# Kernel optimization log

Measured on AMD Instinct MI355X. Metric: run time of the kernel, lower is better.

## Reference

```python
import jax, jax.numpy as jnp
import numpy as np

EPS = 1e-5

def _pw1d(W, b, x):  # W (O,C), x (B,C,N) -> (B,O,N); 1x1 Conv1d
    return jnp.einsum('oc,bcn->bon', W, x) + b[None, :, None]

def _pw2d(W, b, x):  # W (O,C), x (B,C,N,K) -> (B,O,N,K); 1x1 Conv2d
    return jnp.einsum('oc,bcnk->bonk', W, x) + b[None, :, None, None]

def _bn(x, g, b, m, v):  # BatchNorm2d, eval mode, over channel axis 1
    scale = g / jnp.sqrt(v + EPS)
    return (x - m[None, :, None, None]) * scale[None, :, None, None] + b[None, :, None, None]

def _knn(pos, k):  # pos (B,3,N) -> idx (B,N,K) of nearest neighbors (incl. self)
    p = jnp.transpose(pos, (0, 2, 1))             # (B,N,3)
    sq = jnp.sum(p * p, axis=-1)                  # (B,N)
    d = sq[:, :, None] - 2.0 * jnp.einsum('bid,bjd->bij', p, p) + sq[:, None, :]
    _, idx = jax.lax.top_k(-d, k)
    return idx

def _gather(feat, idx):  # feat (B,C,N), idx (B,N,K) -> (B,C,N,K)
    return jax.vmap(lambda f, i: f[:, i])(feat, idx)


def setup_inputs() -> dict:
    key = jax.random.key(0)
    B, C, N, H, AH, K = 4, 64, 4096, 64, 256, 16
    ks = jax.random.split(key, 32)
    s = lambda i, shp, sc=0.05: jax.random.normal(ks[i], shp, dtype=jnp.float32) * sc
    u = lambda i, shp: jax.random.uniform(ks[i], shp, dtype=jnp.float32, minval=0.5, maxval=1.5)
    return {
        'x': jax.random.normal(ks[0], (B, 3, N), dtype=jnp.float32),
        'y': jax.random.normal(ks[1], (B, C, N), dtype=jnp.float32),
        'W_start': s(2, (C, C)), 'b_start': s(3, (C,)),
        'W_key': s(4, (C, C)), 'b_key': s(5, (C,)),
        'W_query': s(6, (C, 3)), 'b_query': s(7, (C,)),
        'P1': s(8, (H, 3)), 'pb1': s(9, (H,)),
        'bn1_g': u(10, (H,)), 'bn1_b': s(11, (H,)), 'bn1_m': s(12, (H,)), 'bn1_v': u(13, (H,)),
        'P2': s(14, (C, H)), 'pb2': s(15, (C,)),
        'A1': s(16, (AH, C)), 'ab1': s(17, (AH,)),
        'bn2_g': u(18, (AH,)), 'bn2_b': s(19, (AH,)), 'bn2_m': s(20, (AH,)), 'bn2_v': u(21, (AH,)),
        'A2': s(22, (C, AH)), 'ab2': s(23, (C,)),
        'W_end': s(24, (C, C)), 'b_end': s(25, (C,)),
        'n_knn': 16,
    }


def reference(x, y, W_start, b_start, W_key, b_key, W_query, b_query,
              P1, pb1, bn1_g, bn1_b, bn1_m, bn1_v, P2, pb2,
              A1, ab1, bn2_g, bn2_b, bn2_m, bn2_v, A2, ab2,
              W_end, b_end, n_knn):
    identity = y
    y1 = _pw1d(W_start, b_start, y)                 # linear_start, (B,C,N)
    idx = _knn(x, n_knn)                            # (B,N,K)
    key = _pw1d(W_key, b_key, y1)
    value = y1
    query = _pw1d(W_query, b_query, x)              # 3 -> C pointwise
    key_g = _gather(key, idx)                       # (B,C,N,K)
    qk_rel = query[..., None] - key_g
    pos_rel = x[..., None] - _gather(x, idx)        # (B,3,N,K)
    pe = _pw2d(P2, pb2, jax.nn.relu(_bn(_pw2d(P1, pb1, pos_rel), bn1_g, bn1_b, bn1_m, bn1_v)))
    attn = _pw2d(A2, ab2, jax.nn.relu(_bn(_pw2d(A1, ab1, qk_rel + pe), bn2_g, bn2_b, bn2_m, bn2_v)))
    attn = jax.nn.softmax(attn, axis=-1)            # softmax over neighbor axis
    val = value[..., None] + pe                     # (B,C,N,K)
    agg = jnp.sum(attn * val, axis=-1)              # einsum 'bcij,bcij->bci'
    out = _pw1d(W_end, b_end, agg) + identity
    return out
```

## Files before the change

### kernel.cpp

```cpp
#include <hip/hip_runtime.h>
#include <hip/hip_bf16.h>

#define BB 4
#define CC 64
#define NN 4096
#define HH 64
#define AH 256
#define KNN 16
#define EPSV 1e-5f

#define KNN_BLKS 2048
#define PF_BLKS 256
#define PP_BLKS 32

typedef __attribute__((ext_vector_type(8))) short short8;
typedef __attribute__((ext_vector_type(4))) short short4v;
typedef __attribute__((ext_vector_type(4))) unsigned short ushort4v;
typedef __attribute__((ext_vector_type(4))) float floatx4;

__device__ __forceinline__ unsigned short f2bf(float f) {
    unsigned u = __float_as_uint(f);
    u += 0x7FFFu + ((u >> 16) & 1u);
    return (unsigned short)(u >> 16);
}
__device__ __forceinline__ float bf2f(unsigned short u) {
    return __uint_as_float(((unsigned)u) << 16);
}
__device__ __forceinline__ unsigned pkbf(float a, float b) {
    __hip_bfloat162 h = __float22bfloat162_rn(make_float2(a, b));
    return *(reinterpret_cast<unsigned*>(&h));
}
__device__ __forceinline__ unsigned long long umin64(unsigned long long a, unsigned long long b) {
    return a < b ? a : b;
}
__device__ __forceinline__ unsigned long long umax64(unsigned long long a, unsigned long long b) {
    return a > b ? a : b;
}
__device__ __forceinline__ unsigned long long shfl_xor_u64(unsigned long long v, int m) {
    int lo = __shfl_xor((int)(unsigned)(v & 0xFFFFFFFFull), m);
    int hi = __shfl_xor((int)(unsigned)(v >> 32), m);
    return ((unsigned long long)(unsigned)hi << 32) | (unsigned)lo;
}
__device__ __forceinline__ unsigned fmono(float d) {
    unsigned u = __float_as_uint(d);
    return ((int)u < 0) ? ~u : (u | 0x80000000u);
}

#define UPITCH 68
#define HPITCH 68

__device__ __forceinline__ short8 lds_frag(const unsigned short* p) {
    short4v lo = *(const short4v*)p;
    short4v hi = *(const short4v*)(p + 4);
    short8 v;
    v[0] = lo[0]; v[1] = lo[1]; v[2] = lo[2]; v[3] = lo[3];
    v[4] = hi[0]; v[5] = hi[1]; v[6] = hi[2]; v[7] = hi[3];
    return v;
}

__global__ __launch_bounds__(256, 3) void fused_prep_knn(
    const float* __restrict__ x, const float* __restrict__ y,
    const float* __restrict__ Ws, const float* __restrict__ bs,
    const float* __restrict__ Wk, const float* __restrict__ bk,
    const float* __restrict__ Wq, const float* __restrict__ bq,
    const float* __restrict__ P1, const float* __restrict__ pb1,
    const float* __restrict__ P2, const float* __restrict__ A1,
    const float* __restrict__ ab1, const float* __restrict__ A2,
    const float* __restrict__ g1, const float* __restrict__ b1v,
    const float* __restrict__ m1, const float* __restrict__ v1,
    const float* __restrict__ g2, const float* __restrict__ b2v,
    const float* __restrict__ m2, const float* __restrict__ v2,
    const float* __restrict__ Wend,
    int* __restrict__ idx_out,
    unsigned short* __restrict__ y1bf, unsigned short* __restrict__ keybf,
    unsigned short* __restrict__ qrybf,
    unsigned short* __restrict__ A1L, unsigned short* __restrict__ A2L,
    unsigned short* __restrict__ P2L, unsigned short* __restrict__ WendL,
    float* __restrict__ P1p, float* __restrict__ ab1f, float* __restrict__ bn2s_c) {
    __shared__ __align__(16) char smem[49152];
    int blk = blockIdx.x;
    int lane = threadIdx.x & 63;
    int w = threadIdx.x >> 6;

    if (blk < KNN_BLKS) {
        float* px = (float*)smem;
        float* py = px + NN;
        float* pz = py + NN;
        unsigned long long* surv = (unsigned long long*)smem;

        int b = blk >> 9;
        int grp = blk & 511;
        const float* xb = x + (size_t)b * 3 * NN;
        for (int i = threadIdx.x; i < NN; i += 256) {
            px[i] = xb[i];
            py[i] = xb[NN + i];
            pz[i] = xb[2 * NN + i];
        }
        __syncthreads();

        int n0 = (grp << 3) + (w << 1);
        float q0x = px[n0], q0y = py[n0], q0z = pz[n0];
        float q1x = px[n0 + 1], q1y = py[n0 + 1], q1z = pz[n0 + 1];
        float q0w = q0x * q0x + q0y * q0y + q0z * q0z;
        float q1w = q1x * q1x + q1y * q1y + q1z * q1z;
        q0x *= -2.f; q0y *= -2.f; q0z *= -2.f;
        q1x *= -2.f; q1y *= -2.f; q1z *= -2.f;

        float d0reg[64], d1reg[64];
        float vmin0 = 3.4e38f, vmin1 = 3.4e38f;
#pragma unroll
        for (int r = 0; r < 16; ++r) {
            int c = r * 64 + lane;
            float4 cx = ((const float4*)px)[c];
            float4 cy = ((const float4*)py)[c];
            float4 cz = ((const float4*)pz)[c];
            float exv[4] = {cx.x, cx.y, cx.z, cx.w};
            float eyv[4] = {cy.x, cy.y, cy.z, cy.w};
            float ezv[4] = {cz.x, cz.y, cz.z, cz.w};
#pragma unroll
            for (int e = 0; e < 4; ++e) {
                float nx = exv[e], ny = eyv[e], nz = ezv[e];
                float nc = nx * nx + ny * ny + nz * nz;
                float d0 = fmaf(q0x, nx, fmaf(q0y, ny, fmaf(q0z, nz, nc + q0w)));
                float d1 = fmaf(q1x, nx, fmaf(q1y, ny, fmaf(q1z, nz, nc + q1w)));
                d0reg[r * 4 + e] = d0;
                d1reg[r * 4 + e] = d1;
                vmin0 = fminf(vmin0, d0);
                vmin1 = fminf(vmin1, d1);
            }
        }

        float T[2];
#pragma unroll
        for (int t = 0; t < 2; ++t) {
            float v = t ? vmin1 : vmin0;
#pragma unroll
            for (int k = 2; k <= 64; k <<= 1) {
#pragma unroll
                for (int j = k >> 1; j > 0; j >>= 1) {
                    float o = __shfl_xor(v, j);
                    bool lower = (lane & j) == 0;
                    bool up = (lane & k) == 0;
                    float mn = fminf(v, o), mx = fmaxf(v, o);
                    v = (lower == up) ? mn : mx;
                }
            }
            T[t] = __shfl(v, 15);
        }
        __syncthreads();

#pragma unroll
        for (int t = 0; t < 2; ++t) {
            float Tt = T[t];
            unsigned long long* buf = surv + (((w << 1) + t) << 7);
            unsigned cnt = 0;
#pragma unroll
            for (int s = 0; s < 64; ++s) {
                float d = t ? d1reg[s] : d0reg[s];
                bool hit = d <= Tt;
                unsigned long long mask = __ballot(hit);
                if (hit) {
                    unsigned off = cnt + (unsigned)__popcll(mask & ((1ull << lane) - 1ull));
                    if (off < 128) {
                        int j = ((s >> 2) * 64 + lane) * 4 + (s & 3);
                        buf[off] = ((unsigned long long)fmono(d) << 32) | (unsigned)j;
                    }
                }
                cnt += (unsigned)__popcll(mask);
            }
            if (cnt > 128) cnt = 128;

            unsigned long long v0 = (lane < (int)cnt) ? buf[lane] : 0xFFFFFFFFFFFFFFFFull;
            if (cnt <= 64) {
#pragma unroll
                for (int k = 2; k <= 64; k <<= 1) {
#pragma unroll
                    for (int j = k >> 1; j > 0; j >>= 1) {
                        bool lower = (lane & j) == 0;
                        bool up = (lane & k) == 0;
                        unsigned long long o0 = shfl_xor_u64(v0, j);
                        v0 = (lower == up) ? umin64(v0, o0) : umax64(v0, o0);
                    }
                }
            } else {
                unsigned long long v1 = (lane + 64 < (int)cnt) ? buf[lane + 64]
                                                               : 0xFFFFFFFFFFFFFFFFull;
#pragma unroll
                for (int k = 2; k <= 128; k <<= 1) {
#pragma unroll
                    for (int j = k >> 1; j > 0; j >>= 1) {
                        if (j >= 64) {
                            unsigned long long lo = umin64(v0, v1), hi = umax64(v0, v1);
                            v0 = lo; v1 = hi;
                        } else {
                            bool lower = (lane & j) == 0;
                            unsigned long long o0 = shfl_xor_u64(v0, j);
                            bool up0 = ((lane & k) == 0);
                            v0 = (lower == up0) ? umin64(v0, o0) : umax64(v0, o0);
                            unsigned long long o1 = shfl_xor_u64(v1, j);
                            bool up1 = (((64 + lane) & k) == 0);
                            v1 = (lower == up1) ? umin64(v1, o1) : umax64(v1, o1);
                        }
                    }
                }
            }
            if (lane < KNN)
                idx_out[((size_t)b * NN + n0 + t) * KNN + lane] =
                    (int)(unsigned)(v0 & 0xFFFFFFFFull);
        }
    } else if (blk < KNN_BLKS + PF_BLKS) {
        unsigned short* tl = (unsigned short*)smem + w * 16 * UPITCH;
        int g4 = (blk - KNN_BLKS) * 4 + w;
        int b = g4 >> 8;
        int n0 = (g4 & 255) << 4;
        int m = lane & 15, quad = lane >> 4;
        size_t ybase = (size_t)b * CC * NN;

        short8 yA[2];
#pragma unroll
        for (int ks = 0; ks < 2; ++ks)
#pragma unroll
            for (int j = 0; j < 8; j += 2) {
                float a = y[ybase + (size_t)(ks * 32 + quad * 8 + j) * NN + n0 + m];
                float bq2 = y[ybase + (size_t)(ks * 32 + quad * 8 + j + 1) * NN + n0 + m];
                ((unsigned*)&yA[ks])[j >> 1] = pkbf(a, bq2);
            }

#pragma unroll
        for (int ot = 0; ot < 4; ++ot) {
            short8 bb0, bb1;
#pragma unroll
            for (int ks = 0; ks < 2; ++ks) {
                const float* wr = Ws + (ot * 16 + m) * CC + ks * 32 + quad * 8;
                float4 lo = *(const float4*)wr;
                float4 hi = *(const float4*)(wr + 4);
                short8 bb;
                ((unsigned*)&bb)[0] = pkbf(lo.x, lo.y);
                ((unsigned*)&bb)[1] = pkbf(lo.z, lo.w);
                ((unsigned*)&bb)[2] = pkbf(hi.x, hi.y);
                ((unsigned*)&bb)[3] = pkbf(hi.z, hi.w);
                if (ks == 0) bb0 = bb; else bb1 = bb;
            }
            floatx4 acc = (floatx4){0.f, 0.f, 0.f, 0.f};
            acc = __builtin_amdgcn_mfma_f32_16x16x32_bf16(yA[0], bb0, acc, 0, 0, 0);
            acc = __builtin_amdgcn_mfma_f32_16x16x32_bf16(yA[1], bb1, acc, 0, 0, 0);
            float bsv = bs[ot * 16 + m];
#pragma unroll
            for (int r = 0; r < 4; r += 2) {
                unsigned p2 = pkbf(acc[r] + bsv, acc[r + 1] + bsv);
                tl[(4 * quad + r) * UPITCH + ot * 16 + m] = (unsigned short)p2;
                tl[(4 * quad + r + 1) * UPITCH + ot * 16 + m] = (unsigned short)(p2 >> 16);
            }
        }
        __syncthreads();

        short8 uA[2];
#pragma unroll
        for (int ks = 0; ks < 2; ++ks)
            uA[ks] = lds_frag(&tl[m * UPITCH + ks * 32 + quad * 8]);

        int p = lane >> 2, ck = lane & 3;
        size_t obase = ((size_t)b * NN + n0 + p) * CC + ck * 16;
#pragma unroll
        for (int s = 0; s < 4; ++s)
            *(ushort4v*)(y1bf + obase + s * 4) =
                *(const ushort4v*)&tl[p * UPITCH + ck * 16 + s * 4];
        __syncthreads();

#pragma unroll
        for (int ot = 0; ot < 4; ++ot) {
            short8 bb0, bb1;
#pragma unroll
            for (int ks = 0; ks < 2; ++ks) {
                const float* wr = Wk + (ot * 16 + m) * CC + ks * 32 + quad * 8;
                float4 lo = *(const float4*)wr;
                float4 hi = *(const float4*)(wr + 4);
                short8 bb;
                ((unsigned*)&bb)[0] = pkbf(lo.x, lo.y);
                ((unsigned*)&bb)[1] = pkbf(lo.z, lo.w);
                ((unsigned*)&bb)[2] = pkbf(hi.x, hi.y);
                ((unsigned*)&bb)[3] = pkbf(hi.z, hi.w);
                if (ks == 0) bb0 = bb; else bb1 = bb;
            }
            floatx4 acc = (floatx4){0.f, 0.f, 0.f, 0.f};
            acc = __builtin_amdgcn_mfma_f32_16x16x32_bf16(uA[0], bb0, acc, 0, 0, 0);
            acc = __builtin_amdgcn_mfma_f32_16x16x32_bf16(uA[1], bb1, acc, 0, 0, 0);
            float bkv = bk[ot * 16 + m];
#pragma unroll
            for (int r = 0; r < 4; r += 2) {
                unsigned p2 = pkbf(acc[r] + bkv, acc[r + 1] + bkv);
                tl[(4 * quad + r) * UPITCH + ot * 16 + m] = (unsigned short)p2;
                tl[(4 * quad + r + 1) * UPITCH + ot * 16 + m] = (unsigned short)(p2 >> 16);
            }
        }
        __syncthreads();
#pragma unroll
        for (int s = 0; s < 4; ++s)
            *(ushort4v*)(keybf + obase + s * 4) =
                *(const ushort4v*)&tl[p * UPITCH + ck * 16 + s * 4];

        float x0 = x[(size_t)(b * 3 + 0) * NN + n0 + p];
        float x1 = x[(size_t)(b * 3 + 1) * NN + n0 + p];
        float x2 = x[(size_t)(b * 3 + 2) * NN + n0 + p];
#pragma unroll
        for (int s = 0; s < 4; ++s) {
            ushort4v pk;
#pragma unroll
            for (int e = 0; e < 4; ++e) {
                int ch = ck * 16 + s * 4 + e;
                pk[e] = f2bf(Wq[3 * ch + 0] * x0 + Wq[3 * ch + 1] * x1 +
                             Wq[3 * ch + 2] * x2 + bq[ch]);
            }
            *(ushort4v*)(qrybf + obase + s * 4) = pk;
        }
    } else {
        int pb = blk - KNN_BLKS - PF_BLKS;
        int t0 = threadIdx.x;
        int t = pb * 256 + t0;
        const int stride = PP_BLKS * 256;
        if (pb == 0) {
            if (t0 < HH) {
                float s = g1[t0] * rsqrtf(v1[t0] + EPSV);
                float c = b1v[t0] - m1[t0] * s;
                P1p[4 * t0 + 0] = P1[3 * t0 + 0] * s;
                P1p[4 * t0 + 1] = P1[3 * t0 + 1] * s;
                P1p[4 * t0 + 2] = P1[3 * t0 + 2] * s;
                P1p[4 * t0 + 3] = pb1[t0] * s + c;
            }
            if (t0 < AH) {
                float s = g2[t0] * rsqrtf(v2[t0] + EPSV);
                bn2s_c[t0] = s;
                ab1f[t0] = ab1[t0] * s + (b2v[t0] - m2[t0] * s);
            }
        }
        for (int i = t; i < 16384; i += stride) {
            int e = i & 7, ln = (i >> 3) & 63, ks = (i >> 9) & 1, ht = i >> 10;
            int m = ln & 15, q = ln >> 4;
            int h = ht * 16 + m;
            float s = g2[h] * rsqrtf(v2[h] + EPSV);
            A1L[i] = f2bf(A1[h * CC + ks * 32 + q * 8 + e] * s);
        }
        for (int i = t; i < 16384; i += stride) {
            int e = i & 7, ln = (i >> 3) & 63, kk = (i >> 9) & 7, nt = i >> 12;
            int m = ln & 15, q = ln >> 4;
            A2L[i] = f2bf(A2[(nt * 16 + m) * AH + kk * 32 + q * 8 + e]);
        }
        for (int i = t; i < 4096; i += stride) {
            int e = i & 7, ln = (i >> 3) & 63, ks = (i >> 9) & 1, nt = i >> 10;
            int m = ln & 15, q = ln >> 4;
            P2L[i] = f2bf(P2[(nt * 16 + m) * HH + ks * 32 + q * 8 + e]);
        }
        for (int i = t; i < 4096; i += stride) {
            int e = i & 7, ln = (i >> 3) & 63, ks = (i >> 9) & 1, wv = i >> 10;
            int m = ln & 15, q = ln >> 4;
            WendL[i] = f2bf(Wend[(wv * 16 + m) * CC + ks * 32 + q * 8 + e]);
        }
    }
}

__global__ __launch_bounds__(256, 3) void attn_mfma(
    const float* __restrict__ x, const float* __restrict__ y,
    const unsigned short* __restrict__ y1bf, const unsigned short* __restrict__ keybf,
    const unsigned short* __restrict__ qrybf, const int* __restrict__ idx,
    const float* __restrict__ P1p, const unsigned short* __restrict__ P2L,
    const float* __restrict__ pb2, const unsigned short* __restrict__ A1L,
    const float* __restrict__ ab1f, const float* __restrict__ bn2s_c,
    const unsigned short* __restrict__ A2L, const unsigned short* __restrict__ WendL,
    const float* __restrict__ bend,
    float* __restrict__ out) {
    __shared__ unsigned short u_lds[128 * UPITCH];
    __shared__ unsigned short hid_lds[128 * HPITCH];
    __shared__ float agg_lds[8 * 68];
    __shared__ float outstage[512];

    int blk = blockIdx.x;
    int b = blk & 3;
    int n0 = (blk >> 2) << 3;
    int w = threadIdx.x >> 6;
    int lane = threadIdx.x & 63;
    int m = lane & 15, quad = lane >> 4;

    int pt[2];
    size_t bpt[2];
#pragma unroll
    for (int t = 0; t < 2; ++t) {
        pt[t] = n0 + 2 * w + t;
        bpt[t] = (size_t)b * NN + pt[t];
    }

    int jm[2], j4[2][4];
    unsigned short qu[2][4], kvu[2][4][4], y1u[2][4];
#pragma unroll
    for (int t = 0; t < 2; ++t) {
        jm[t] = idx[bpt[t] * KNN + m];
#pragma unroll
        for (int r = 0; r < 4; ++r) j4[t][r] = idx[bpt[t] * KNN + 4 * quad + r];
#pragma unroll
        for (int nt = 0; nt < 4; ++nt) {
            qu[t][nt] = qrybf[bpt[t] * CC + nt * 16 + m];
            y1u[t][nt] = y1bf[bpt[t] * CC + nt * 16 + m];
#pragma unroll
            for (int r = 0; r < 4; ++r)
                kvu[t][nt][r] = keybf[((size_t)b * NN + j4[t][r]) * CC + nt * 16 + m];
        }
    }

    short8 h1A[2][2];
#pragma unroll
    for (int t = 0; t < 2; ++t) {
        float dx = x[(size_t)(b * 3 + 0) * NN + pt[t]] - x[(size_t)(b * 3 + 0) * NN + jm[t]];
        float dy = x[(size_t)(b * 3 + 1) * NN + pt[t]] - x[(size_t)(b * 3 + 1) * NN + jm[t]];
        float dz = x[(size_t)(b * 3 + 2) * NN + pt[t]] - x[(size_t)(b * 3 + 2) * NN + jm[t]];
#pragma unroll
        for (int ks = 0; ks < 2; ++ks)
#pragma unroll
            for (int j = 0; j < 8; j += 2) {
                int h1 = ks * 32 + quad * 8 + j;
                const float4 p0 = *(const float4*)(P1p + 4 * h1);
                const float4 p1 = *(const float4*)(P1p + 4 * h1 + 4);
                float a0 = fmaxf(p0.x * dx + p0.y * dy + p0.z * dz + p0.w, 0.f);
                float a1 = fmaxf(p1.x * dx + p1.y * dy + p1.z * dz + p1.w, 0.f);
                ((unsigned*)&h1A[t][ks])[j >> 1] = pkbf(a0, a1);
            }
    }

    floatx4 pacc[2][4];
#pragma unroll
    for (int t = 0; t < 2; ++t)
#pragma unroll
        for (int nt = 0; nt < 4; ++nt) pacc[t][nt] = (floatx4){0.f, 0.f, 0.f, 0.f};
#pragma unroll
    for (int ks = 0; ks < 2; ++ks)
#pragma unroll
        for (int nt = 0; nt < 4; ++nt) {
            short8 bb = *(const short8*)(P2L + ((nt * 2 + ks) * 64 + lane) * 8);
            pacc[0][nt] = __builtin_amdgcn_mfma_f32_16x16x32_bf16(h1A[0][ks], bb, pacc[0][nt], 0, 0, 0);
            pacc[1][nt] = __builtin_amdgcn_mfma_f32_16x16x32_bf16(h1A[1][ks], bb, pacc[1][nt], 0, 0, 0);
        }
#pragma unroll
    for (int nt = 0; nt < 4; ++nt) {
        float pb = pb2[nt * 16 + m];
#pragma unroll
        for (int t = 0; t < 2; ++t)
#pragma unroll
            for (int r = 0; r < 4; ++r) pacc[t][nt][r] += pb;
    }

#pragma unroll
    for (int t = 0; t < 2; ++t)
#pragma unroll
        for (int nt = 0; nt < 4; ++nt) {
            float qv = bf2f(qu[t][nt]);
            float u0 = qv - bf2f(kvu[t][nt][0]) + pacc[t][nt][0];
            float u1 = qv - bf2f(kvu[t][nt][1]) + pacc[t][nt][1];
            float u2 = qv - bf2f(kvu[t][nt][2]) + pacc[t][nt][2];
            float u3 = qv - bf2f(kvu[t][nt][3]) + pacc[t][nt][3];
            unsigned p01 = pkbf(u0, u1), p23 = pkbf(u2, u3);
            int base = (w * 32 + t * 16 + 4 * quad) * UPITCH + nt * 16 + m;
            u_lds[base + 0 * UPITCH] = (unsigned short)p01;
            u_lds[base + 1 * UPITCH] = (unsigned short)(p01 >> 16);
            u_lds[base + 2 * UPITCH] = (unsigned short)p23;
            u_lds[base + 3 * UPITCH] = (unsigned short)(p23 >> 16);
        }

    short8 uA[2][2];
#pragma unroll
    for (int t = 0; t < 2; ++t)
#pragma unroll
        for (int ks = 0; ks < 2; ++ks)
            uA[t][ks] = lds_frag(&u_lds[(w * 32 + t * 16 + m) * UPITCH + ks * 32 + quad * 8]);

    floatx4 acc2[2][4];
#pragma unroll
    for (int t = 0; t < 2; ++t)
#pragma unroll
        for (int nt = 0; nt < 4; ++nt) acc2[t][nt] = (floatx4){0.f, 0.f, 0.f, 0.f};

    for (int qd = 0; qd < 4; ++qd) {
#pragma unroll
        for (int nt4 = 0; nt4 < 4; ++nt4) {
            int ht = qd * 4 + nt4;
            const unsigned short* a1t = A1L + ht * 1024 + lane * 8;
            short8 b0 = *(const short8*)(a1t);
            short8 b1 = *(const short8*)(a1t + 512);
            int h = ht * 16 + m;
            float t0 = ab1f[h];
#pragma unroll
            for (int t = 0; t < 2; ++t) {
                floatx4 acc = (floatx4){0.f, 0.f, 0.f, 0.f};
                acc = __builtin_amdgcn_mfma_f32_16x16x32_bf16(uA[t][0], b0, acc, 0, 0, 0);
                acc = __builtin_amdgcn_mfma_f32_16x16x32_bf16(uA[t][1], b1, acc, 0, 0, 0);
                float h0 = fmaxf(acc[0] + t0, 0.f);
                float h1 = fmaxf(acc[1] + t0, 0.f);
                float h2 = fmaxf(acc[2] + t0, 0.f);
                float h3 = fmaxf(acc[3] + t0, 0.f);
                unsigned p01 = pkbf(h0, h1), p23 = pkbf(h2, h3);
                int base = (w * 32 + t * 16 + 4 * quad) * HPITCH + nt4 * 16 + m;
                hid_lds[base + 0 * HPITCH] = (unsigned short)p01;
                hid_lds[base + 1 * HPITCH] = (unsigned short)(p01 >> 16);
                hid_lds[base + 2 * HPITCH] = (unsigned short)p23;
                hid_lds[base + 3 * HPITCH] = (unsigned short)(p23 >> 16);
            }
        }
        short8 hA[2][2];
#pragma unroll
        for (int t = 0; t < 2; ++t)
#pragma unroll
            for (int ks = 0; ks < 2; ++ks)
                hA[t][ks] = lds_frag(&hid_lds[(w * 32 + t * 16 + m) * HPITCH + ks * 32 + quad * 8]);
#pragma unroll
        for (int ks = 0; ks < 2; ++ks)
#pragma unroll
            for (int nt = 0; nt < 4; ++nt) {
                int kk = qd * 2 + ks;
                short8 bb = *(const short8*)(A2L + ((nt * 8 + kk) * 64 + lane) * 8);
                acc2[0][nt] = __builtin_amdgcn_mfma_f32_16x16x32_bf16(hA[0][ks], bb, acc2[0][nt], 0, 0, 0);
                acc2[1][nt] = __builtin_amdgcn_mfma_f32_16x16x32_bf16(hA[1][ks], bb, acc2[1][nt], 0, 0, 0);
            }
    }

#pragma unroll
    for (int t = 0; t < 2; ++t)
#pragma unroll
        for (int nt = 0; nt < 4; ++nt) {
            float l0 = acc2[t][nt][0], l1 = acc2[t][nt][1];
            float l2 = acc2[t][nt][2], l3 = acc2[t][nt][3];
            float mx = fmaxf(fmaxf(l0, l1), fmaxf(l2, l3));
            mx = fmaxf(mx, __shfl_xor(mx, 16));
            mx = fmaxf(mx, __shfl_xor(mx, 32));
            float e0 = __expf(l0 - mx), e1 = __expf(l1 - mx);
            float e2 = __expf(l2 - mx), e3 = __expf(l3 - mx);
            float sum = (e0 + e1) + (e2 + e3);
            sum += __shfl_xor(sum, 16);
            sum += __shfl_xor(sum, 32);
            float y1v = bf2f(y1u[t][nt]);
            float contrib = e0 * (y1v + pacc[t][nt][0]) + e1 * (y1v + pacc[t][nt][1]) +
                            e2 * (y1v + pacc[t][nt][2]) + e3 * (y1v + pacc[t][nt][3]);
            contrib += __shfl_xor(contrib, 16);
            contrib += __shfl_xor(contrib, 32);
            float agg = contrib / sum;
            if (quad == 0) agg_lds[(2 * w + t) * 68 + nt * 16 + m] = agg;
        }
    __syncthreads();

    short8 aggA[2];
#pragma unroll
    for (int ks = 0; ks < 2; ++ks)
#pragma unroll
        for (int j = 0; j < 8; j += 2) {
            float a0 = agg_lds[(m & 7) * 68 + ks * 32 + quad * 8 + j];
            float a1 = agg_lds[(m & 7) * 68 + ks * 32 + quad * 8 + j + 1];
            ((unsigned*)&aggA[ks])[j >> 1] = pkbf(a0, a1);
        }
    short8 wb0 = *(const short8*)(WendL + ((w * 2 + 0) * 64 + lane) * 8);
    short8 wb1 = *(const short8*)(WendL + ((w * 2 + 1) * 64 + lane) * 8);
    floatx4 facc = (floatx4){0.f, 0.f, 0.f, 0.f};
    facc = __builtin_amdgcn_mfma_f32_16x16x32_bf16(aggA[0], wb0, facc, 0, 0, 0);
    facc = __builtin_amdgcn_mfma_f32_16x16x32_bf16(aggA[1], wb1, facc, 0, 0, 0);
    if (quad < 2) {
        float be = bend[w * 16 + m];
#pragma unroll
        for (int r = 0; r < 4; ++r)
            outstage[(w * 16 + m) * 8 + 4 * quad + r] = facc[r] + be;
    }
    __syncthreads();

    int t2 = threadIdx.x;
    int o = t2 >> 2, pp = (t2 & 3) * 2;
#pragma unroll
    for (int e = 0; e < 2; ++e) {
        size_t oi = ((size_t)(b * CC + o)) * NN + n0 + pp + e;
        out[oi] = outstage[o * 8 + pp + e] + y[oi];
    }
}

extern "C" void kernel_launch(void* const* d_in, const int* in_sizes, int n_in,
                              void* d_out, int out_size, void* d_ws, size_t ws_size,
                              hipStream_t stream) {
    const float* x    = (const float*)d_in[0];
    const float* y    = (const float*)d_in[1];
    const float* Ws   = (const float*)d_in[2];
    const float* bs   = (const float*)d_in[3];
    const float* Wk   = (const float*)d_in[4];
    const float* bk   = (const float*)d_in[5];
    const float* Wq   = (const float*)d_in[6];
    const float* bq   = (const float*)d_in[7];
    const float* P1   = (const float*)d_in[8];
    const float* pb1  = (const float*)d_in[9];
    const float* g1   = (const float*)d_in[10];
    const float* b1   = (const float*)d_in[11];
    const float* m1   = (const float*)d_in[12];
    const float* v1   = (const float*)d_in[13];
    const float* P2   = (const float*)d_in[14];
    const float* pb2  = (const float*)d_in[15];
    const float* A1   = (const float*)d_in[16];
    const float* ab1  = (const float*)d_in[17];
    const float* g2   = (const float*)d_in[18];
    const float* b2   = (const float*)d_in[19];
    const float* m2   = (const float*)d_in[20];
    const float* v2   = (const float*)d_in[21];
    const float* A2   = (const float*)d_in[22];
    const float* ab2  = (const float*)d_in[23];
    const float* Wend = (const float*)d_in[24];
    const float* bend = (const float*)d_in[25];
    (void)ab2;

    unsigned short* usws = (unsigned short*)d_ws;
    unsigned short* y1bf  = usws;
    unsigned short* keybf = usws + 1048576;
    unsigned short* qrybf = usws + 2097152;
    int* idx = (int*)(usws + 3145728);
    unsigned short* A1L = usws + 3670016;
    unsigned short* A2L = A1L + 16384;
    unsigned short* P2L = A2L + 16384;
    unsigned short* WendL = P2L + 4096;
    float* P1p   = (float*)(WendL + 4096);
    float* ab1f  = P1p + 256;
    float* bn2sc = ab1f + 256;
    float* out   = (float*)d_out;

    hipLaunchKernelGGL(fused_prep_knn, dim3(KNN_BLKS + PF_BLKS + PP_BLKS), dim3(256), 0, stream,
                       x, y, Ws, bs, Wk, bk, Wq, bq,
                       P1, pb1, P2, A1, ab1, A2,
                       g1, b1, m1, v1, g2, b2, m2, v2, Wend,
                       idx, y1bf, keybf, qrybf,
                       A1L, A2L, P2L, WendL, P1p, ab1f, bn2sc);
    hipLaunchKernelGGL(attn_mfma, dim3(2048), dim3(256), 0, stream,
                       x, y, y1bf, keybf, qrybf, idx,
                       P1p, P2L, pb2, A1L, ab1f, bn2sc, A2L, WendL,
                       bend, out);
}
```

Before: 195.4 us.

## Interleave channel layout for vectorized neighbor gathers and fold log2e into softmax

Stores y1, key and query in a permuted channel order (g*4+nt holds channel nt*16+g). Each lane's four channels become contiguous, so the attention kernel gathers neighbor keys and loads query and y1 with one 8-byte vector load instead of four scalar 2-byte loads. This targets the cost of the random-access key gather. Separately, it pre-scales A2 by log2(e) so the softmax can use exp2f directly; the per-channel bias cancels over the neighbor axis, so the result is unchanged. The risk is that any unseen consumer of these buffers that assumes the old channel order would now read wrong data.

```diff
diff --git a/kernel.cpp b/kernel.cpp
--- a/kernel.cpp
+++ b/kernel.cpp
@@ -8,6 +8,7 @@
 #define AH 256
 #define KNN 16
 #define EPSV 1e-5f
+#define LOG2E 1.44269504088896f
 
 #define KNN_BLKS 2048
 #define PF_BLKS 256
@@ -57,6 +58,7 @@
     v[4] = hi[0]; v[5] = hi[1]; v[6] = hi[2]; v[7] = hi[3];
     return v;
 }
+
 
 __global__ __launch_bounds__(256, 3) void fused_prep_knn(
     const float* __restrict__ x, const float* __restrict__ y,
@@ -259,12 +261,17 @@
         for (int ks = 0; ks < 2; ++ks)
             uA[ks] = lds_frag(&tl[m * UPITCH + ks * 32 + quad * 8]);
 
-        int p = lane >> 2, ck = lane & 3;
-        size_t obase = ((size_t)b * NN + n0 + p) * CC + ck * 16;
-#pragma unroll
-        for (int s = 0; s < 4; ++s)
-            *(ushort4v*)(y1bf + obase + s * 4) =
-                *(const ushort4v*)&tl[p * UPITCH + ck * 16 + s * 4];
+        int p = lane >> 2, gb = lane & 3;
+        size_t obase = ((size_t)b * NN + n0 + p) * 64;
+#pragma unroll
+        for (int s = 0; s < 4; ++s) {
+            int g = gb * 4 + s;
+            ushort4v pk;
+#pragma unroll
+            for (int nt = 0; nt < 4; ++nt)
+                pk[nt] = tl[p * UPITCH + nt * 16 + g];
+            *(ushort4v*)(y1bf + obase + g * 4) = pk;
+        }
         __syncthreads();
 
 #pragma unroll
@@ -295,23 +302,29 @@
         }
         __syncthreads();
 #pragma unroll
-        for (int s = 0; s < 4; ++s)
-            *(ushort4v*)(keybf + obase + s * 4) =
-                *(const ushort4v*)&tl[p * UPITCH + ck * 16 + s * 4];
+        for (int s = 0; s < 4; ++s) {
+            int g = gb * 4 + s;
+            ushort4v pk;
+#pragma unroll
+            for (int nt = 0; nt < 4; ++nt)
+                pk[nt] = tl[p * UPITCH + nt * 16 + g];
+            *(ushort4v*)(keybf + obase + g * 4) = pk;
+        }
 
         float x0 = x[(size_t)(b * 3 + 0) * NN + n0 + p];
         float x1 = x[(size_t)(b * 3 + 1) * NN + n0 + p];
         float x2 = x[(size_t)(b * 3 + 2) * NN + n0 + p];
 #pragma unroll
         for (int s = 0; s < 4; ++s) {
+            int g = gb * 4 + s;
             ushort4v pk;
 #pragma unroll
-            for (int e = 0; e < 4; ++e) {
-                int ch = ck * 16 + s * 4 + e;
-                pk[e] = f2bf(Wq[3 * ch + 0] * x0 + Wq[3 * ch + 1] * x1 +
-                             Wq[3 * ch + 2] * x2 + bq[ch]);
-            }
-            *(ushort4v*)(qrybf + obase + s * 4) = pk;
+            for (int nt = 0; nt < 4; ++nt) {
+                int ch = nt * 16 + g;
+                pk[nt] = f2bf(Wq[3 * ch + 0] * x0 + Wq[3 * ch + 1] * x1 +
+                              Wq[3 * ch + 2] * x2 + bq[ch]);
+            }
+            *(ushort4v*)(qrybf + obase + g * 4) = pk;
         }
     } else {
         int pb = blk - KNN_BLKS - PF_BLKS;
@@ -343,7 +356,7 @@
         for (int i = t; i < 16384; i += stride) {
             int e = i & 7, ln = (i >> 3) & 63, kk = (i >> 9) & 7, nt = i >> 12;
             int m = ln & 15, q = ln >> 4;
-            A2L[i] = f2bf(A2[(nt * 16 + m) * AH + kk * 32 + q * 8 + e]);
+            A2L[i] = f2bf(A2[(nt * 16 + m) * AH + kk * 32 + q * 8 + e] * LOG2E);
         }
         for (int i = t; i < 4096; i += stride) {
             int e = i & 7, ln = (i >> 3) & 63, ks = (i >> 9) & 1, nt = i >> 10;
@@ -389,20 +402,17 @@
     }
 
     int jm[2], j4[2][4];
-    unsigned short qu[2][4], kvu[2][4][4], y1u[2][4];
+    ushort4v qu4[2], y14[2], kv4[2][4];
 #pragma unroll
     for (int t = 0; t < 2; ++t) {
         jm[t] = idx[bpt[t] * KNN + m];
 #pragma unroll
         for (int r = 0; r < 4; ++r) j4[t][r] = idx[bpt[t] * KNN + 4 * quad + r];
-#pragma unroll
-        for (int nt = 0; nt < 4; ++nt) {
-            qu[t][nt] = qrybf[bpt[t] * CC + nt * 16 + m];
-            y1u[t][nt] = y1bf[bpt[t] * CC + nt * 16 + m];
-#pragma unroll
-            for (int r = 0; r < 4; ++r)
-                kvu[t][nt][r] = keybf[((size_t)b * NN + j4[t][r]) * CC + nt * 16 + m];
-        }
+        qu4[t] = *(const ushort4v*)(qrybf + bpt[t] * 64 + m * 4);
+        y14[t] = *(const ushort4v*)(y1bf + bpt[t] * 64 + m * 4);
+#pragma unroll
+        for (int r = 0; r < 4; ++r)
+            kv4[t][r] = *(const ushort4v*)(keybf + ((size_t)b * NN + j4[t][r]) * 64 + m * 4);
     }
 
     short8 h1A[2][2];
@@ -450,11 +460,11 @@
     for (int t = 0; t < 2; ++t)
 #pragma unroll
         for (int nt = 0; nt < 4; ++nt) {
-            float qv = bf2f(qu[t][nt]);
-            float u0 = qv - bf2f(kvu[t][nt][0]) + pacc[t][nt][0];
-            float u1 = qv - bf2f(kvu[t][nt][1]) + pacc[t][nt][1];
-            float u2 = qv - bf2f(kvu[t][nt][2]) + pacc[t][nt][2];
-            float u3 = qv - bf2f(kvu[t][nt][3]) + pacc[t][nt][3];
+            float qv = bf2f(qu4[t][nt]);
+            float u0 = qv - bf2f(kv4[t][0][nt]) + pacc[t][nt][0];
+            float u1 = qv - bf2f(kv4[t][1][nt]) + pacc[t][nt][1];
+            float u2 = qv - bf2f(kv4[t][2][nt]) + pacc[t][nt][2];
+            float u3 = qv - bf2f(kv4[t][3][nt]) + pacc[t][nt][3];
             unsigned p01 = pkbf(u0, u1), p23 = pkbf(u2, u3);
             int base = (w * 32 + t * 16 + 4 * quad) * UPITCH + nt * 16 + m;
             u_lds[base + 0 * UPITCH] = (unsigned short)p01;
@@ -528,12 +538,12 @@
             float mx = fmaxf(fmaxf(l0, l1), fmaxf(l2, l3));
             mx = fmaxf(mx, __shfl_xor(mx, 16));
             mx = fmaxf(mx, __shfl_xor(mx, 32));
-            float e0 = __expf(l0 - mx), e1 = __expf(l1 - mx);
-            float e2 = __expf(l2 - mx), e3 = __expf(l3 - mx);
+            float e0 = exp2f(l0 - mx), e1 = exp2f(l1 - mx);
+            float e2 = exp2f(l2 - mx), e3 = exp2f(l3 - mx);
             float sum = (e0 + e1) + (e2 + e3);
             sum += __shfl_xor(sum, 16);
             sum += __shfl_xor(sum, 32);
-            float y1v = bf2f(y1u[t][nt]);
+            float y1v = bf2f(y14[t][nt]);
             float contrib = e0 * (y1v + pacc[t][nt][0]) + e1 * (y1v + pacc[t][nt][1]) +
                             e2 * (y1v + pacc[t][nt][2]) + e3 * (y1v + pacc[t][nt][3]);
             contrib += __shfl_xor(contrib, 16);
```

After: 195.3 us. No clear change (-0.1%).
